# Kernel optimization log

Measured on AMD Instinct MI355X. Metric: run time of the kernel, lower is better.

The kernel has to match this reference:

```python
import jax, jax.numpy as jnp
import numpy as np

C = 2.0 + 1e-6
_nodes, _weights = np.polynomial.laguerre.laggauss(2)
QUAD_NODES = jnp.asarray(np.maximum(_nodes, 0.01) / C, dtype=jnp.float32)
QUAD_WEIGHTS = jnp.asarray(np.maximum(_weights, 0.01) / C, dtype=jnp.float32)
H, HD, P, M = 4, 64, 16, 32  # heads, head_dim, poly_dim, num_features
NUM_LABELS = 131072


def safe_normalize(x, axis=-1, eps=1e-4):
    n = jnp.linalg.norm(x, axis=axis, keepdims=True)
    return x / jnp.maximum(n, eps)


def safe_log(x, eps=1e-8):
    return jnp.log(jnp.maximum(x, eps))


def slay_features(x, omega, anchors):
    # x: [N, H*HD]; omega: [R,H,HD,M] (pre-scaled); anchors: [P,HD] (unit-norm)
    N = x.shape[0]
    xr = safe_normalize(x.reshape(N, H, HD), axis=-1)
    poly_proj = jnp.clip(jnp.einsum('nhd,pd->nhp', xr, anchors), -1.0, 1.0)
    poly_feat = poly_proj ** 2 / np.float32(np.sqrt(P))          # [N,H,P]
    prf_proj = jnp.einsum('nhd,rhdm->rnhm', xr, omega)           # [R,N,H,M]
    s = jnp.maximum(QUAD_NODES, 1e-6).reshape(-1, 1, 1, 1)
    exp_arg = jnp.clip(prf_proj * jnp.sqrt(2.0 * s) - s, -20.0, 20.0)
    prf_feat = jnp.exp(exp_arg) / np.float32(np.sqrt(M + 1e-6))
    prf_feat = prf_feat * jnp.sqrt(jnp.maximum(QUAD_WEIGHTS, 1e-6)).reshape(-1, 1, 1, 1)
    # fuse poly x prf, concat over quadrature nodes r (r-major feature order)
    fused = poly_feat[None, :, :, :, None] * prf_feat[:, :, :, None, :]  # [R,N,H,P,M]
    return fused.transpose(1, 0, 2, 3, 4).reshape(N, -1)         # [N, R*H*P*M]


def setup_inputs() -> dict:
    key = jax.random.key(0)
    ks = jax.random.split(key, 9)
    B, L, K = 1024, 128, 8
    return {
        'indices': jax.random.randint(ks[0], (B, L), 0, 100000),
        'mask': jnp.ones((B, L), dtype=jnp.float32),
        'labels': jax.random.randint(ks[1], (B, K), 0, NUM_LABELS),
        'label_mask': jnp.ones((B, K), dtype=jnp.float32),
        'neg_indices': jax.random.randint(ks[2], (2048,), 0, NUM_LABELS),
        'embed_table': jax.random.normal(ks[3], (100000, 256), dtype=jnp.float32),
        'kernel': jax.random.normal(ks[4], (256, NUM_LABELS), dtype=jnp.float32),
        'omega': jax.random.normal(ks[5], (2, H, HD, M), dtype=jnp.float32),
        'anchors': jax.random.normal(ks[6], (P, HD), dtype=jnp.float32),
    }


def reference(indices, mask, labels, label_mask, neg_indices, embed_table, kernel, omega, anchors):
    B, K = labels.shape
    # init-time parameter normalizations from the module
    omega_n = omega / np.float32(np.sqrt(HD))
    anchors_n = anchors / jnp.linalg.norm(anchors, axis=-1, keepdims=True)
    # MeanEmbedding encoder
    embeds = embed_table[indices]                                 # [B,L,D]
    summed = jnp.sum(embeds * mask[:, :, None], axis=1)
    query = summed / jnp.maximum(jnp.sum(mask, axis=1, keepdims=True), 1.0)
    query = safe_normalize(query, axis=-1)
    phi_query = slay_features(query, omega_n, anchors_n)          # [B,F]
    # sampled classifier rows
    W = safe_normalize(kernel.T, axis=-1)                         # [num_labels,D]
    safe_labels = jnp.maximum(labels, 0)
    all_needed = jnp.concatenate([safe_labels.reshape(-1), neg_indices])  # [B*K+Nneg]
    W_subset = W[all_needed]
    phi_W = slay_features(W_subset, omega_n, anchors_n)           # [B*K+Nneg,F]
    scores = phi_query @ phi_W.T                                  # [B, B*K+Nneg]
    idx_offsets = jnp.arange(B)[:, None] * K + jnp.arange(K)[None, :]
    pos_scores = jnp.take_along_axis(scores, idx_offsets, axis=1) # [B,K]
    neg_scores = scores[:, B * K:]                                # [B,Nneg]
    all_scores = jnp.concatenate([pos_scores, neg_scores], axis=1) + 1e-8
    log_Z = jax.scipy.special.logsumexp(safe_log(all_scores), axis=1)
    log_probs = safe_log(pos_scores + 1e-8) - log_Z[:, None]
    return -jnp.sum(log_probs * label_mask) / (jnp.sum(label_mask) + 1e-6)
```

## Files before the change

### kernel.cpp

```cpp
#include <hip/hip_runtime.h>
#include <math.h>

#define B_Q 1024
#define L_SEQ 128
#define D_EMB 256
#define NLAB 131072
#define LBL_ROWS 8192
#define NEG_ROWS 2048
#define W_ROWS 10240
#define CROW 320
#define LST 82
#define RPB 32
#define SXS 258

__device__ __forceinline__ float wave_sum(float v) {
#pragma unroll
  for (int off = 32; off > 0; off >>= 1) v += __shfl_xor(v, off, 64);
  return v;
}

__device__ __forceinline__ void slay_tail(const float* __restrict__ sx, int t,
                                          const float* __restrict__ anchT,
                                          const float* __restrict__ omega,
                                          float* __restrict__ outrow) {
  if (t < 64) {
    const int h = t >> 4, p = t & 15;
    const float* x = sx + h * 64;
    float d = 0.f;
#pragma unroll
    for (int dd = 0; dd < 64; dd++) d = fmaf(x[dd], anchT[dd * 16 + p], d);
    d = fminf(fmaxf(d, -1.0f), 1.0f);
    outrow[h * 16 + p] = d * d * 0.25f;
  }
  {
    const int r = t >> 7;
    const int h = (t >> 5) & 3;
    const float* x = sx + h * 64;
    const float* om = omega + (size_t)(t >> 5) * 2048 + (t & 31);
    float d = 0.f;
#pragma unroll
    for (int dd = 0; dd < 64; dd++) d = fmaf(x[dd], om[dd * 32], d);
    const float proj = d * 0.125f;
    const float s = r ? 1.70710592763316f : 0.29289307236691f;
    const float w = r ? 0.07322326809171f : 0.42677648190829f;
    float arg = proj * sqrtf(2.0f * s) - s;
    arg = fminf(fmaxf(arg, -20.0f), 20.0f);
    outrow[64 + t] = expf(arg) * (sqrtf(w) / sqrtf(32.000001f));
  }
}

__global__ __launch_bounds__(256) void k_setup(const float* __restrict__ anchors,
                                               const int* __restrict__ labels,
                                               const int* __restrict__ negidx,
                                               float* __restrict__ anchT,
                                               float* __restrict__ negparts,
                                               int* __restrict__ jidx,
                                               int* __restrict__ sorted) {
  __shared__ int shist[2048];
  __shared__ int s2[256];
  const int t = threadIdx.x, bx = blockIdx.x;
  if (bx == 0) {
    if (t < 64) {
      for (int p = 0; p < 16; p++) {
        const float v = anchors[p * 64 + t];
        const float n = sqrtf(wave_sum(v * v));
        anchT[t * 16 + p] = v / n;
      }
    }
  } else if (bx <= 256) {
    negparts[(bx - 1) * 256 + t] = 0.f;
  } else {
    for (int i = t; i < 2048; i += 256) shist[i] = 0;
    __syncthreads();
    int4 lv[8], nv[2];
#pragma unroll
    for (int e = 0; e < 8; e++) {
      int4 v = ((const int4*)labels)[e * 256 + t];
      v.x = max(v.x, 0); v.y = max(v.y, 0); v.z = max(v.z, 0); v.w = max(v.w, 0);
      lv[e] = v;
      ((int4*)jidx)[e * 256 + t] = v;
      atomicAdd(&shist[v.x >> 6], 1); atomicAdd(&shist[v.y >> 6], 1);
      atomicAdd(&shist[v.z >> 6], 1); atomicAdd(&shist[v.w >> 6], 1);
    }
#pragma unroll
    for (int e = 0; e < 2; e++) {
      const int4 v = ((const int4*)negidx)[e * 256 + t];
      nv[e] = v;
      ((int4*)jidx)[2048 + e * 256 + t] = v;
      atomicAdd(&shist[v.x >> 6], 1); atomicAdd(&shist[v.y >> 6], 1);
      atomicAdd(&shist[v.z >> 6], 1); atomicAdd(&shist[v.w >> 6], 1);
    }
    __syncthreads();
    int v[8]; int sum = 0;
#pragma unroll
    for (int e = 0; e < 8; e++) { v[e] = shist[t * 8 + e]; sum += v[e]; }
    s2[t] = sum; __syncthreads();
    for (int off = 1; off < 256; off <<= 1) {
      const int x = s2[t];
      const int y = (t >= off) ? s2[t - off] : 0;
      __syncthreads();
      s2[t] = x + y;
      __syncthreads();
    }
    int run = s2[t] - sum;
#pragma unroll
    for (int e = 0; e < 8; e++) { shist[t * 8 + e] = run; run += v[e]; }
    __syncthreads();
#pragma unroll
    for (int e = 0; e < 8; e++) {
      const int i = (e * 256 + t) * 4;
      sorted[atomicAdd(&shist[lv[e].x >> 6], 1)] = i;
      sorted[atomicAdd(&shist[lv[e].y >> 6], 1)] = i + 1;
      sorted[atomicAdd(&shist[lv[e].z >> 6], 1)] = i + 2;
      sorted[atomicAdd(&shist[lv[e].w >> 6], 1)] = i + 3;
    }
#pragma unroll
    for (int e = 0; e < 2; e++) {
      const int i = LBL_ROWS + (e * 256 + t) * 4;
      sorted[atomicAdd(&shist[nv[e].x >> 6], 1)] = i;
      sorted[atomicAdd(&shist[nv[e].y >> 6], 1)] = i + 1;
      sorted[atomicAdd(&shist[nv[e].z >> 6], 1)] = i + 2;
      sorted[atomicAdd(&shist[nv[e].w >> 6], 1)] = i + 3;
    }
  }
}

__global__ __launch_bounds__(256, 4) void k_feat(const int* __restrict__ indices,
                                                 const float* __restrict__ mask,
                                                 const float* __restrict__ embed,
                                                 const float* __restrict__ kern,
                                                 const float* __restrict__ anchT,
                                                 const float* __restrict__ omega,
                                                 const int* __restrict__ jidx,
                                                 const int* __restrict__ sorted,
                                                 float* __restrict__ qcomp,
                                                 float* __restrict__ wcomp) {
  __shared__ __align__(16) float smem[9504];
  const int tid = threadIdx.x;

  if (blockIdx.x < B_Q) {
    const int b = blockIdx.x, t = tid;
    const int wv = t >> 6, ln = t & 63;
    int* sidx = (int*)smem;
    float* smask = smem + 128;
    float4* spart = (float4*)(smem + 256);
    float* smsum = smem + 1280;
    float* sx = smem + 1296;
    if (t < L_SEQ) { sidx[t] = indices[b * L_SEQ + t]; smask[t] = mask[b * L_SEQ + t]; }
    __syncthreads();
    float4 acc = {0.f, 0.f, 0.f, 0.f};
    float msum = 0.f;
#pragma unroll 8
    for (int l = wv * 32; l < wv * 32 + 32; l++) {
      const float m = smask[l];
      msum += m;
      const float4 e = *(const float4*)(embed + (size_t)sidx[l] * D_EMB + ln * 4);
      acc.x = fmaf(e.x, m, acc.x); acc.y = fmaf(e.y, m, acc.y);
      acc.z = fmaf(e.z, m, acc.z); acc.w = fmaf(e.w, m, acc.w);
    }
    spart[wv * 64 + ln] = acc;
    if (ln == 0) smsum[wv] = msum;
    __syncthreads();
    const float* spf = (const float*)spart;
    float q = spf[t] + spf[256 + t] + spf[512 + t] + spf[768 + t];
    const float mt = smsum[0] + smsum[1] + smsum[2] + smsum[3];
    q /= fmaxf(mt, 1.0f);
    const float ss = wave_sum(q * q);
    sx[t] = q / fmaxf(sqrtf(ss), 1e-4f);
    __syncthreads();
    slay_tail(sx, t, anchT, omega, qcomp + (size_t)b * CROW);
  } else {
    const int lb = blockIdx.x - B_Q;
    int* sj = (int*)smem;
    int* ssid = (int*)smem + 32;
    float* rnorm = smem + 64;
    float* sq = smem + 192;
    float* sx = smem + 1248;
    const int cb = (lb & 7) * 40 + (lb >> 3);
    const int i0 = cb * RPB;

    if (tid < RPB) {
      const int sid = sorted[i0 + tid];
      ssid[tid] = sid;
      sj[tid] = jidx[sid];
    }
    __syncthreads();

    {
      const int row = tid & 31, dloc = tid >> 5;
      const float* kbase = kern + ((size_t)dloc << 17) + (size_t)sj[row];
      float ssq[4] = {0.f, 0.f, 0.f, 0.f};
#pragma unroll
      for (int it = 0; it < 32; it++) {
        const float v = kbase[(size_t)it << 20];
        sx[row * SXS + it * 8 + dloc] = v;
        ssq[it >> 3] = fmaf(v, v, ssq[it >> 3]);
      }
#pragma unroll
      for (int h = 0; h < 4; h++) sq[row * 33 + dloc * 4 + h] = ssq[h];
    }
    __syncthreads();
    if (tid < 128) {
      const int r2 = tid >> 2, h = tid & 3;
      float s = 0.f;
#pragma unroll
      for (int dl = 0; dl < 8; dl++) s += sq[r2 * 33 + dl * 4 + h];
      rnorm[r2 * 4 + h] = 1.0f / fmaxf(sqrtf(s), 1e-4f);
    }
    __syncthreads();

    {
      const int hh = (tid >> 5) & 3, r = tid >> 7;
      const float* om = omega + (size_t)(tid >> 5) * 2048 + (tid & 31);
      const float s = r ? 1.70710592763316f : 0.29289307236691f;
      const float w = r ? 0.07322326809171f : 0.42677648190829f;
      const float sc = sqrtf(2.0f * s);
      const float outs = sqrtf(w) / sqrtf(32.000001f);
#pragma unroll
      for (int half = 0; half < 2; half++) {
        float acc[16];
#pragma unroll
        for (int rq = 0; rq < 16; rq++) acc[rq] = 0.f;
#pragma unroll
        for (int dd = 0; dd < 64; dd += 2) {
          const float o0 = om[dd * 32], o1 = om[dd * 32 + 32];
#pragma unroll
          for (int rq = 0; rq < 16; rq++) {
            const float2 xv = *(const float2*)(sx + (half * 16 + rq) * SXS + hh * 64 + dd);
            acc[rq] = fmaf(xv.x, o0, fmaf(xv.y, o1, acc[rq]));
          }
        }
#pragma unroll
        for (int rq = 0; rq < 16; rq++) {
          const int row = half * 16 + rq;
          float arg = acc[rq] * 0.125f * rnorm[row * 4 + hh] * sc - s;
          arg = fminf(fmaxf(arg, -20.0f), 20.0f);
          wcomp[(size_t)ssid[row] * CROW + 64 + tid] = expf(arg) * outs;
        }
      }
    }

    {
      const int hp = tid & 63, rp = tid >> 6;
      const int h = hp >> 4, p = hp & 15;
#pragma unroll
      for (int pr = 0; pr < 4; pr++) {
        const int r0 = rp * 8 + pr * 2;
        const float* x0 = sx + r0 * SXS + h * 64;
        const float* x1 = x0 + SXS;
        float d0 = 0.f, d1 = 0.f;
#pragma unroll
        for (int dd = 0; dd < 64; dd++) {
          const float a = anchT[dd * 16 + p];
          d0 = fmaf(x0[dd], a, d0);
          d1 = fmaf(x1[dd], a, d1);
        }
        d0 *= rnorm[r0 * 4 + h];
        d1 *= rnorm[(r0 + 1) * 4 + h];
        d0 = fminf(fmaxf(d0, -1.0f), 1.0f);
        d1 = fminf(fmaxf(d1, -1.0f), 1.0f);
        wcomp[(size_t)ssid[r0] * CROW + h * 16 + p]     = d0 * d0 * 0.25f;
        wcomp[(size_t)ssid[r0 + 1] * CROW + h * 16 + p] = d1 * d1 * 0.25f;
      }
    }
  }
}

__global__ __launch_bounds__(128) void k_score(const float* __restrict__ qcomp,
                                               const float* __restrict__ wcomp,
                                               float* __restrict__ negparts,
                                               float* __restrict__ pos) {
  __shared__ float qt[64 * LST];
  __shared__ float wt[32 * LST];
  const int tid = threadIdx.x;

  if (blockIdx.x < 4096) {
    const int qb0 = (blockIdx.x & 15) * 64;
    const int wb  = (blockIdx.x >> 4) & 63;
    const int wr0 = LBL_ROWS + wb * 32;
    const int h   = blockIdx.x >> 10;

    for (int idx = tid; idx < 96 * 20; idx += 128) {
      const int row = idx / 20, c4 = idx % 20;
      int col, lcol;
      if (c4 < 4)       { col = h * 16 + c4 * 4;              lcol = c4 * 4; }
      else if (c4 < 12) { col = 64 + h * 32 + (c4 - 4) * 4;   lcol = 16 + (c4 - 4) * 4; }
      else              { col = 192 + h * 32 + (c4 - 12) * 4; lcol = 48 + (c4 - 12) * 4; }
      const bool isq = row < 64;
      const int grow = isq ? (qb0 + row) : (wr0 + row - 64);
      const float4 v = *(const float4*)((isq ? qcomp : wcomp) + (size_t)grow * CROW + col);
      float* dst = (isq ? qt + row * LST : wt + (row - 64) * LST) + lcol;
      dst[0] = v.x; dst[1] = v.y; dst[2] = v.z; dst[3] = v.w;
    }
    __syncthreads();

    const int qg = tid >> 3;
    const int wg = tid & 7;
    const float* qb = qt + (qg * 4) * LST;
    const float* wbp = wt + (wg * 4) * LST;

    float pd[4][4] = {{0.f}}, pf[4][4] = {{0.f}};
#pragma unroll
    for (int kc = 0; kc < 8; kc++) {
      float2 qv[4], wv[4];
#pragma unroll
      for (int i = 0; i < 4; i++) qv[i] = *(const float2*)(qb + i * LST + 2 * kc);
#pragma unroll
      for (int j = 0; j < 4; j++) wv[j] = *(const float2*)(wbp + j * LST + 2 * kc);
#pragma unroll
      for (int i = 0; i < 4; i++)
#pragma unroll
        for (int j = 0; j < 4; j++) {
          pd[i][j] = fmaf(qv[i].x, wv[j].x, pd[i][j]);
          pd[i][j] = fmaf(qv[i].y, wv[j].y, pd[i][j]);
        }
    }
#pragma unroll 8
    for (int kc = 0; kc < 32; kc++) {
      float2 qv[4], wv[4];
#pragma unroll
      for (int i = 0; i < 4; i++) qv[i] = *(const float2*)(qb + i * LST + 16 + 2 * kc);
#pragma unroll
      for (int j = 0; j < 4; j++) wv[j] = *(const float2*)(wbp + j * LST + 16 + 2 * kc);
#pragma unroll
      for (int i = 0; i < 4; i++)
#pragma unroll
        for (int j = 0; j < 4; j++) {
          pf[i][j] = fmaf(qv[i].x, wv[j].x, pf[i][j]);
          pf[i][j] = fmaf(qv[i].y, wv[j].y, pf[i][j]);
        }
    }

#pragma unroll
    for (int i = 0; i < 4; i++) {
      float acc = 0.f;
#pragma unroll
      for (int j = 0; j < 4; j++) acc += pd[i][j] * pf[i][j];
#pragma unroll
      for (int off = 1; off < 8; off <<= 1) acc += __shfl_xor(acc, off, 64);
      if (wg == 0) atomicAdd(&negparts[wb * B_Q + qb0 + qg * 4 + i], acc);
    }
  } else {
    const int g = (blockIdx.x - 4096) * 32 + (tid >> 2);
    const int h = tid & 3;
    const float* q = qcomp + (size_t)(g >> 3) * CROW;
    const float* w = wcomp + (size_t)g * CROW;
    float pd = 0.f, pf = 0.f;
#pragma unroll
    for (int c = 0; c < 4; c++) {
      const float4 qv = *(const float4*)(q + h * 16 + c * 4);
      const float4 wv = *(const float4*)(w + h * 16 + c * 4);
      pd += qv.x * wv.x + qv.y * wv.y + qv.z * wv.z + qv.w * wv.w;
    }
#pragma unroll
    for (int r = 0; r < 2; r++)
#pragma unroll
      for (int c = 0; c < 8; c++) {
        const float4 qv = *(const float4*)(q + 64 + r * 128 + h * 32 + c * 4);
        const float4 wv = *(const float4*)(w + 64 + r * 128 + h * 32 + c * 4);
        pf += qv.x * wv.x + qv.y * wv.y + qv.z * wv.z + qv.w * wv.w;
      }
    float sc = pd * pf;
    sc += __shfl_xor(sc, 1, 64);
    sc += __shfl_xor(sc, 2, 64);
    if (h == 0) pos[g] = sc;
  }
}

__global__ __launch_bounds__(1024) void k_loss(const float* __restrict__ pos,
                                               const float* __restrict__ negparts,
                                               const float* __restrict__ lmask,
                                               float* __restrict__ out) {
  const int b = threadIdx.x;
  float lp[8];
  float possum = 0.f;
#pragma unroll
  for (int k = 0; k < 8; k++) { lp[k] = pos[b * 8 + k]; possum += lp[k]; }
  float negsum = 0.f;
#pragma unroll 8
  for (int c = 0; c < 64; c++) negsum += negparts[c * B_Q + b];
  const float Z = possum + negsum + 2.056e-5f;
  const float logZ = logf(Z);
  float local = 0.f, lsum = 0.f;
#pragma unroll
  for (int k = 0; k < 8; k++) {
    const float lm = lmask[b * 8 + k];
    local += lm * (logf(lp[k] + 1e-8f) - logZ);
    lsum += lm;
  }
  local = wave_sum(local);
  lsum = wave_sum(lsum);
  __shared__ float r1[16], r2[16];
  const int wid = b >> 6;
  if ((b & 63) == 0) { r1[wid] = local; r2[wid] = lsum; }
  __syncthreads();
  if (b == 0) {
    float t1 = 0.f, t2 = 0.f;
    for (int wv = 0; wv < 16; wv++) { t1 += r1[wv]; t2 += r2[wv]; }
    out[0] = -t1 / (t2 + 1e-6f);
  }
}

extern "C" void kernel_launch(void* const* d_in, const int* in_sizes, int n_in,
                              void* d_out, int out_size, void* d_ws, size_t ws_size,
                              hipStream_t stream) {
  const int* indices  = (const int*)d_in[0];
  const float* mask   = (const float*)d_in[1];
  const int* labels   = (const int*)d_in[2];
  const float* lmask  = (const float*)d_in[3];
  const int* negidx   = (const int*)d_in[4];
  const float* embed  = (const float*)d_in[5];
  const float* kern   = (const float*)d_in[6];
  const float* omega  = (const float*)d_in[7];
  const float* anchors= (const float*)d_in[8];
  float* out = (float*)d_out;

  float* ws = (float*)d_ws;
  float* anchT    = ws;
  float* qcomp    = anchT + 1024;
  float* wcomp    = qcomp + (size_t)B_Q * CROW;
  float* pos      = wcomp + (size_t)W_ROWS * CROW;
  float* negparts = pos + LBL_ROWS;
  int*   jidx     = (int*)(negparts + 64 * B_Q);
  int*   sorted   = jidx + W_ROWS;

  k_setup<<<258, 256, 0, stream>>>(anchors, labels, negidx, anchT, negparts, jidx, sorted);
  k_feat<<<B_Q + W_ROWS / RPB, 256, 0, stream>>>(indices, mask, embed, kern, anchT, omega,
                                                 jidx, sorted, qcomp, wcomp);
  k_score<<<4096 + 256, 128, 0, stream>>>(qcomp, wcomp, negparts, pos);
  k_loss<<<1, 1024, 0, stream>>>(pos, negparts, lmask, out);
}
```

Measured before the change: 355.2 us.

## Stream full classifier kernel coalesced and scatter needed columns into a compact buffer

The old fused setup and feature kernels are split into a prep/mark/scan/scatter pipeline that builds a label-to-slot map, deduplicating repeated labels with atomicMin. A new gather kernel reads the whole 256x131072 kernel matrix with coalesced float4 loads and scatters only the needed columns into a dense W_ROWS-wide buffer. The projection kernel then reads from that compact buffer instead of issuing strided 4-byte gathers across the large matrix. The aim is to replace latency-bound scattered reads with sequential bandwidth-bound streaming. In exchange it reads the entire matrix and adds several extra kernel launches plus workspace for the gathered columns and slot map.

Measured after the change: 391.5 us. 10.2% more time.

```diff
diff --git a/kernel.cpp b/kernel.cpp
--- a/kernel.cpp
+++ b/kernel.cpp
@@ -12,6 +12,7 @@
 #define LST 82
 #define RPB 32
 #define SXS 258
+#define SLOT_EMPTY 0x7FFFFFFF
 
 __device__ __forceinline__ float wave_sum(float v) {
 #pragma unroll
@@ -49,15 +50,11 @@
   }
 }
 
-__global__ __launch_bounds__(256) void k_setup(const float* __restrict__ anchors,
-                                               const int* __restrict__ labels,
-                                               const int* __restrict__ negidx,
-                                               float* __restrict__ anchT,
-                                               float* __restrict__ negparts,
-                                               int* __restrict__ jidx,
-                                               int* __restrict__ sorted) {
-  __shared__ int shist[2048];
-  __shared__ int s2[256];
+__global__ __launch_bounds__(256) void k_prep(const float* __restrict__ anchors,
+                                              float* __restrict__ anchT,
+                                              float* __restrict__ negparts,
+                                              int* __restrict__ hist,
+                                              int* __restrict__ slotmap) {
   const int t = threadIdx.x, bx = blockIdx.x;
   if (bx == 0) {
     if (t < 64) {
@@ -69,77 +66,85 @@
     }
   } else if (bx <= 256) {
     negparts[(bx - 1) * 256 + t] = 0.f;
+  } else if (bx <= 264) {
+    hist[(bx - 257) * 256 + t] = 0;
   } else {
-    for (int i = t; i < 2048; i += 256) shist[i] = 0;
-    __syncthreads();
-    int4 lv[8], nv[2];
-#pragma unroll
-    for (int e = 0; e < 8; e++) {
-      int4 v = ((const int4*)labels)[e * 256 + t];
-      v.x = max(v.x, 0); v.y = max(v.y, 0); v.z = max(v.z, 0); v.w = max(v.w, 0);
-      lv[e] = v;
-      ((int4*)jidx)[e * 256 + t] = v;
-      atomicAdd(&shist[v.x >> 6], 1); atomicAdd(&shist[v.y >> 6], 1);
-      atomicAdd(&shist[v.z >> 6], 1); atomicAdd(&shist[v.w >> 6], 1);
-    }
-#pragma unroll
-    for (int e = 0; e < 2; e++) {
-      const int4 v = ((const int4*)negidx)[e * 256 + t];
-      nv[e] = v;
-      ((int4*)jidx)[2048 + e * 256 + t] = v;
-      atomicAdd(&shist[v.x >> 6], 1); atomicAdd(&shist[v.y >> 6], 1);
-      atomicAdd(&shist[v.z >> 6], 1); atomicAdd(&shist[v.w >> 6], 1);
-    }
-    __syncthreads();
-    int v[8]; int sum = 0;
-#pragma unroll
-    for (int e = 0; e < 8; e++) { v[e] = shist[t * 8 + e]; sum += v[e]; }
-    s2[t] = sum; __syncthreads();
-    for (int off = 1; off < 256; off <<= 1) {
-      const int x = s2[t];
-      const int y = (t >= off) ? s2[t - off] : 0;
-      __syncthreads();
-      s2[t] = x + y;
-      __syncthreads();
-    }
-    int run = s2[t] - sum;
-#pragma unroll
-    for (int e = 0; e < 8; e++) { shist[t * 8 + e] = run; run += v[e]; }
-    __syncthreads();
-#pragma unroll
-    for (int e = 0; e < 8; e++) {
-      const int i = (e * 256 + t) * 4;
-      sorted[atomicAdd(&shist[lv[e].x >> 6], 1)] = i;
-      sorted[atomicAdd(&shist[lv[e].y >> 6], 1)] = i + 1;
-      sorted[atomicAdd(&shist[lv[e].z >> 6], 1)] = i + 2;
-      sorted[atomicAdd(&shist[lv[e].w >> 6], 1)] = i + 3;
-    }
-#pragma unroll
-    for (int e = 0; e < 2; e++) {
-      const int i = LBL_ROWS + (e * 256 + t) * 4;
-      sorted[atomicAdd(&shist[nv[e].x >> 6], 1)] = i;
-      sorted[atomicAdd(&shist[nv[e].y >> 6], 1)] = i + 1;
-      sorted[atomicAdd(&shist[nv[e].z >> 6], 1)] = i + 2;
-      sorted[atomicAdd(&shist[nv[e].w >> 6], 1)] = i + 3;
-    }
-  }
-}
-
-__global__ __launch_bounds__(256, 4) void k_feat(const int* __restrict__ indices,
-                                                 const float* __restrict__ mask,
-                                                 const float* __restrict__ embed,
-                                                 const float* __restrict__ kern,
-                                                 const float* __restrict__ anchT,
-                                                 const float* __restrict__ omega,
-                                                 const int* __restrict__ jidx,
-                                                 const int* __restrict__ sorted,
-                                                 float* __restrict__ qcomp,
-                                                 float* __restrict__ wcomp) {
-  __shared__ __align__(16) float smem[9504];
+    slotmap[(bx - 265) * 256 + t] = SLOT_EMPTY;
+  }
+}
+
+__global__ __launch_bounds__(256) void k_mark(const int* __restrict__ labels,
+                                              const int* __restrict__ negidx,
+                                              int* __restrict__ jidx,
+                                              int* __restrict__ hist) {
+  const int i = blockIdx.x * 256 + threadIdx.x;
+  if (i >= W_ROWS) return;
+  int j;
+  if (i < LBL_ROWS) { j = labels[i]; if (j < 0) j = 0; }
+  else               { j = negidx[i - LBL_ROWS]; }
+  jidx[i] = j;
+  atomicAdd(&hist[j >> 6], 1);
+}
+
+__global__ __launch_bounds__(256) void k_scan(int* __restrict__ hist) {
+  __shared__ int s[256];
+  const int t = threadIdx.x;
+  int v[8]; int sum = 0;
+#pragma unroll
+  for (int e = 0; e < 8; e++) { v[e] = hist[t * 8 + e]; sum += v[e]; }
+  s[t] = sum; __syncthreads();
+  for (int off = 1; off < 256; off <<= 1) {
+    const int x = s[t];
+    const int y = (t >= off) ? s[t - off] : 0;
+    __syncthreads();
+    s[t] = x + y;
+    __syncthreads();
+  }
+  int run = s[t] - sum;
+#pragma unroll
+  for (int e = 0; e < 8; e++) { hist[t * 8 + e] = run; run += v[e]; }
+}
+
+__global__ __launch_bounds__(256) void k_scatter(const int* __restrict__ jidx,
+                                                 int* __restrict__ hist,
+                                                 int* __restrict__ sorted,
+                                                 int* __restrict__ slotmap) {
+  const int i = blockIdx.x * 256 + threadIdx.x;
+  if (i >= W_ROWS) return;
+  const int j = jidx[i];
+  const int pos = atomicAdd(&hist[j >> 6], 1);
+  sorted[pos] = i;
+  atomicMin(&slotmap[j], pos);
+}
+
+__global__ __launch_bounds__(256) void k_gather(const float* __restrict__ kern,
+                                                const int* __restrict__ slotmap,
+                                                float* __restrict__ wgath,
+                                                const int* __restrict__ indices,
+                                                const float* __restrict__ mask,
+                                                const float* __restrict__ embed,
+                                                const float* __restrict__ anchT,
+                                                const float* __restrict__ omega,
+                                                float* __restrict__ qcomp) {
   const int tid = threadIdx.x;
-
-  if (blockIdx.x < B_Q) {
-    const int b = blockIdx.x, t = tid;
+  if (blockIdx.x < 2048) {
+    const int d = blockIdx.x >> 3, chunk = blockIdx.x & 7;
+    const float4* kb = (const float4*)(kern + ((size_t)d << 17)) + chunk * 4096;
+    const int4* sm = (const int4*)slotmap + chunk * 4096;
+    float* wg = wgath + (size_t)d * W_ROWS;
+#pragma unroll 4
+    for (int it = 0; it < 16; it++) {
+      const int idx = it * 256 + tid;
+      const float4 v = kb[idx];
+      const int4 s = sm[idx];
+      if (s.x < W_ROWS) wg[s.x] = v.x;
+      if (s.y < W_ROWS) wg[s.y] = v.y;
+      if (s.z < W_ROWS) wg[s.z] = v.z;
+      if (s.w < W_ROWS) wg[s.w] = v.w;
+    }
+  } else {
+    __shared__ __align__(16) float smem[1552];
+    const int b = blockIdx.x - 2048, t = tid;
     const int wv = t >> 6, ln = t & 63;
     int* sidx = (int*)smem;
     float* smask = smem + 128;
@@ -169,99 +174,112 @@
     sx[t] = q / fmaxf(sqrtf(ss), 1e-4f);
     __syncthreads();
     slay_tail(sx, t, anchT, omega, qcomp + (size_t)b * CROW);
-  } else {
-    const int lb = blockIdx.x - B_Q;
-    int* sj = (int*)smem;
-    int* ssid = (int*)smem + 32;
-    float* rnorm = smem + 64;
-    float* sq = smem + 192;
-    float* sx = smem + 1248;
-    const int cb = (lb & 7) * 40 + (lb >> 3);
-    const int i0 = cb * RPB;
-
-    if (tid < RPB) {
-      const int sid = sorted[i0 + tid];
-      ssid[tid] = sid;
-      sj[tid] = jidx[sid];
-    }
-    __syncthreads();
-
-    {
-      const int row = tid & 31, dloc = tid >> 5;
-      const float* kbase = kern + ((size_t)dloc << 17) + (size_t)sj[row];
-      float ssq[4] = {0.f, 0.f, 0.f, 0.f};
-#pragma unroll
-      for (int it = 0; it < 32; it++) {
-        const float v = kbase[(size_t)it << 20];
-        sx[row * SXS + it * 8 + dloc] = v;
-        ssq[it >> 3] = fmaf(v, v, ssq[it >> 3]);
-      }
-#pragma unroll
-      for (int h = 0; h < 4; h++) sq[row * 33 + dloc * 4 + h] = ssq[h];
-    }
-    __syncthreads();
-    if (tid < 128) {
-      const int r2 = tid >> 2, h = tid & 3;
-      float s = 0.f;
-#pragma unroll
-      for (int dl = 0; dl < 8; dl++) s += sq[r2 * 33 + dl * 4 + h];
-      rnorm[r2 * 4 + h] = 1.0f / fmaxf(sqrtf(s), 1e-4f);
-    }
-    __syncthreads();
-
-    {
-      const int hh = (tid >> 5) & 3, r = tid >> 7;
-      const float* om = omega + (size_t)(tid >> 5) * 2048 + (tid & 31);
-      const float s = r ? 1.70710592763316f : 0.29289307236691f;
-      const float w = r ? 0.07322326809171f : 0.42677648190829f;
-      const float sc = sqrtf(2.0f * s);
-      const float outs = sqrtf(w) / sqrtf(32.000001f);
-#pragma unroll
-      for (int half = 0; half < 2; half++) {
-        float acc[16];
-#pragma unroll
-        for (int rq = 0; rq < 16; rq++) acc[rq] = 0.f;
-#pragma unroll
-        for (int dd = 0; dd < 64; dd += 2) {
-          const float o0 = om[dd * 32], o1 = om[dd * 32 + 32];
-#pragma unroll
-          for (int rq = 0; rq < 16; rq++) {
-            const float2 xv = *(const float2*)(sx + (half * 16 + rq) * SXS + hh * 64 + dd);
-            acc[rq] = fmaf(xv.x, o0, fmaf(xv.y, o1, acc[rq]));
-          }
-        }
+  }
+}
+
+__global__ __launch_bounds__(256) void k_wproj(const int* __restrict__ sorted,
+                                               const int* __restrict__ jidx,
+                                               const int* __restrict__ slotmap,
+                                               const float* __restrict__ wgath,
+                                               const float* __restrict__ anchT,
+                                               const float* __restrict__ omega,
+                                               float* __restrict__ wcomp) {
+  __shared__ __align__(16) float smem[9536];
+  int* sj = (int*)smem;
+  int* ssid = (int*)smem + 32;
+  int* sslot = (int*)smem + 64;
+  float* rnorm = smem + 96;
+  float* sq = smem + 224;
+  float* sx = smem + 1280;
+  const int tid = threadIdx.x;
+  const int lb = blockIdx.x;
+  const int cb = (lb & 7) * 40 + (lb >> 3);
+  const int i0 = cb * RPB;
+
+  if (tid < RPB) {
+    const int sid = sorted[i0 + tid];
+    ssid[tid] = sid;
+    const int j = jidx[sid];
+    sj[tid] = j;
+    sslot[tid] = slotmap[j];
+  }
+  __syncthreads();
+
+  {
+    const int row = tid & 31, dloc = tid >> 5;
+    const float* wg = wgath + sslot[row];
+    float ssq[4] = {0.f, 0.f, 0.f, 0.f};
+#pragma unroll
+    for (int it = 0; it < 32; it++) {
+      const float v = wg[(size_t)(it * 8 + dloc) * W_ROWS];
+      sx[row * SXS + it * 8 + dloc] = v;
+      ssq[it >> 3] = fmaf(v, v, ssq[it >> 3]);
+    }
+#pragma unroll
+    for (int h = 0; h < 4; h++) sq[row * 33 + dloc * 4 + h] = ssq[h];
+  }
+  __syncthreads();
+  if (tid < 128) {
+    const int r2 = tid >> 2, h = tid & 3;
+    float s = 0.f;
+#pragma unroll
+    for (int dl = 0; dl < 8; dl++) s += sq[r2 * 33 + dl * 4 + h];
+    rnorm[r2 * 4 + h] = 1.0f / fmaxf(sqrtf(s), 1e-4f);
+  }
+  __syncthreads();
+
+  {
+    const int hh = (tid >> 5) & 3, r = tid >> 7;
+    const float* om = omega + (size_t)(tid >> 5) * 2048 + (tid & 31);
+    const float s = r ? 1.70710592763316f : 0.29289307236691f;
+    const float w = r ? 0.07322326809171f : 0.42677648190829f;
+    const float sc = sqrtf(2.0f * s);
+    const float outs = sqrtf(w) / sqrtf(32.000001f);
+#pragma unroll
+    for (int half = 0; half < 2; half++) {
+      float acc[16];
+#pragma unroll
+      for (int rq = 0; rq < 16; rq++) acc[rq] = 0.f;
+#pragma unroll
+      for (int dd = 0; dd < 64; dd += 2) {
+        const float o0 = om[dd * 32], o1 = om[dd * 32 + 32];
 #pragma unroll
         for (int rq = 0; rq < 16; rq++) {
-          const int row = half * 16 + rq;
-          float arg = acc[rq] * 0.125f * rnorm[row * 4 + hh] * sc - s;
-          arg = fminf(fmaxf(arg, -20.0f), 20.0f);
-          wcomp[(size_t)ssid[row] * CROW + 64 + tid] = expf(arg) * outs;
+          const float2 xv = *(const float2*)(sx + (half * 16 + rq) * SXS + hh * 64 + dd);
+          acc[rq] = fmaf(xv.x, o0, fmaf(xv.y, o1, acc[rq]));
         }
       }
-    }
-
-    {
-      const int hp = tid & 63, rp = tid >> 6;
-      const int h = hp >> 4, p = hp & 15;
-#pragma unroll
-      for (int pr = 0; pr < 4; pr++) {
-        const int r0 = rp * 8 + pr * 2;
-        const float* x0 = sx + r0 * SXS + h * 64;
-        const float* x1 = x0 + SXS;
-        float d0 = 0.f, d1 = 0.f;
-#pragma unroll
-        for (int dd = 0; dd < 64; dd++) {
-          const float a = anchT[dd * 16 + p];
-          d0 = fmaf(x0[dd], a, d0);
-          d1 = fmaf(x1[dd], a, d1);
-        }
-        d0 *= rnorm[r0 * 4 + h];
-        d1 *= rnorm[(r0 + 1) * 4 + h];
-        d0 = fminf(fmaxf(d0, -1.0f), 1.0f);
-        d1 = fminf(fmaxf(d1, -1.0f), 1.0f);
-        wcomp[(size_t)ssid[r0] * CROW + h * 16 + p]     = d0 * d0 * 0.25f;
-        wcomp[(size_t)ssid[r0 + 1] * CROW + h * 16 + p] = d1 * d1 * 0.25f;
+#pragma unroll
+      for (int rq = 0; rq < 16; rq++) {
+        const int row = half * 16 + rq;
+        float arg = acc[rq] * 0.125f * rnorm[row * 4 + hh] * sc - s;
+        arg = fminf(fmaxf(arg, -20.0f), 20.0f);
+        wcomp[(size_t)ssid[row] * CROW + 64 + tid] = expf(arg) * outs;
       }
+    }
+  }
+
+  {
+    const int hp = tid & 63, rp = tid >> 6;
+    const int h = hp >> 4, p = hp & 15;
+#pragma unroll
+    for (int pr = 0; pr < 4; pr++) {
+      const int r0 = rp * 8 + pr * 2;
+      const float* x0 = sx + r0 * SXS + h * 64;
+      const float* x1 = x0 + SXS;
+      float d0 = 0.f, d1 = 0.f;
+#pragma unroll
+      for (int dd = 0; dd < 64; dd++) {
+        const float a = anchT[dd * 16 + p];
+        d0 = fmaf(x0[dd], a, d0);
+        d1 = fmaf(x1[dd], a, d1);
+      }
+      d0 *= rnorm[r0 * 4 + h];
+      d1 *= rnorm[(r0 + 1) * 4 + h];
+      d0 = fminf(fmaxf(d0, -1.0f), 1.0f);
+      d1 = fminf(fmaxf(d1, -1.0f), 1.0f);
+      wcomp[(size_t)ssid[r0] * CROW + h * 16 + p]     = d0 * d0 * 0.25f;
+      wcomp[(size_t)ssid[r0 + 1] * CROW + h * 16 + p] = d1 * d1 * 0.25f;
     }
   }
 }
@@ -419,14 +437,21 @@
   float* anchT    = ws;
   float* qcomp    = anchT + 1024;
   float* wcomp    = qcomp + (size_t)B_Q * CROW;
-  float* pos      = wcomp + (size_t)W_ROWS * CROW;
+  float* wgath    = wcomp + (size_t)W_ROWS * CROW;
+  float* pos      = wgath + (size_t)D_EMB * W_ROWS;
   float* negparts = pos + LBL_ROWS;
   int*   jidx     = (int*)(negparts + 64 * B_Q);
   int*   sorted   = jidx + W_ROWS;
-
-  k_setup<<<258, 256, 0, stream>>>(anchors, labels, negidx, anchT, negparts, jidx, sorted);
-  k_feat<<<B_Q + W_ROWS / RPB, 256, 0, stream>>>(indices, mask, embed, kern, anchT, omega,
-                                                 jidx, sorted, qcomp, wcomp);
+  int*   hist     = sorted + W_ROWS;
+  int*   slotmap  = hist + 2048;
+
+  k_prep<<<777, 256, 0, stream>>>(anchors, anchT, negparts, hist, slotmap);
+  k_mark<<<40, 256, 0, stream>>>(labels, negidx, jidx, hist);
+  k_scan<<<1, 256, 0, stream>>>(hist);
+  k_scatter<<<40, 256, 0, stream>>>(jidx, hist, sorted, slotmap);
+  k_gather<<<3072, 256, 0, stream>>>(kern, slotmap, wgath, indices, mask, embed,
+                                     anchT, omega, qcomp);
+  k_wproj<<<W_ROWS / RPB, 256, 0, stream>>>(sorted, jidx, slotmap, wgath, anchT, omega, wcomp);
   k_score<<<4096 + 256, 128, 0, stream>>>(qcomp, wcomp, negparts, pos);
   k_loss<<<1, 1024, 0, stream>>>(pos, negparts, lmask, out);
 }
```

## Retile negative scoring to 128x64 blocks looping heads, dropping atomics

Applied to the files above, without the earlier changes.

The negative-score kernel now uses 256-thread blocks that each cover 128 queries by 64 negative rows and loop over all four heads inside the block. Each thread keeps an 8x4 register tile, and the W tile is stored transposed in shared memory. Per-head products are accumulated in registers, so each partial is written with a plain store instead of an atomicAdd, and the zero-fill of negparts in setup is removed. The goal is more data reuse and register blocking, plus fewer launches and atomics, at the cost of a much smaller grid (384 blocks) and higher register pressure.

New measurement: 357.1 us. Within noise of the previous version (+0.6%).

```diff
diff --git a/kernel.cpp b/kernel.cpp
--- a/kernel.cpp
+++ b/kernel.cpp
@@ -9,9 +9,10 @@
 #define NEG_ROWS 2048
 #define W_ROWS 10240
 #define CROW 320
-#define LST 82
 #define RPB 32
 #define SXS 258
+#define QST 84
+#define NWT 32
 
 __device__ __forceinline__ float wave_sum(float v) {
 #pragma unroll
@@ -53,7 +54,6 @@
                                                const int* __restrict__ labels,
                                                const int* __restrict__ negidx,
                                                float* __restrict__ anchT,
-                                               float* __restrict__ negparts,
                                                int* __restrict__ jidx,
                                                int* __restrict__ sorted) {
   __shared__ int shist[2048];
@@ -67,8 +67,6 @@
         anchT[t * 16 + p] = v / n;
       }
     }
-  } else if (bx <= 256) {
-    negparts[(bx - 1) * 256 + t] = 0.f;
   } else {
     for (int i = t; i < 2048; i += 256) shist[i] = 0;
     __syncthreads();
@@ -266,82 +264,110 @@
   }
 }
 
-__global__ __launch_bounds__(128) void k_score(const float* __restrict__ qcomp,
+__global__ __launch_bounds__(256) void k_score(const float* __restrict__ qcomp,
                                                const float* __restrict__ wcomp,
                                                float* __restrict__ negparts,
                                                float* __restrict__ pos) {
-  __shared__ float qt[64 * LST];
-  __shared__ float wt[32 * LST];
+  __shared__ __align__(16) float sq[128 * QST];
+  __shared__ __align__(16) float swt[80 * 64];
   const int tid = threadIdx.x;
 
-  if (blockIdx.x < 4096) {
-    const int qb0 = (blockIdx.x & 15) * 64;
-    const int wb  = (blockIdx.x >> 4) & 63;
-    const int wr0 = LBL_ROWS + wb * 32;
-    const int h   = blockIdx.x >> 10;
-
-    for (int idx = tid; idx < 96 * 20; idx += 128) {
-      const int row = idx / 20, c4 = idx % 20;
-      int col, lcol;
-      if (c4 < 4)       { col = h * 16 + c4 * 4;              lcol = c4 * 4; }
-      else if (c4 < 12) { col = 64 + h * 32 + (c4 - 4) * 4;   lcol = 16 + (c4 - 4) * 4; }
-      else              { col = 192 + h * 32 + (c4 - 12) * 4; lcol = 48 + (c4 - 12) * 4; }
-      const bool isq = row < 64;
-      const int grow = isq ? (qb0 + row) : (wr0 + row - 64);
-      const float4 v = *(const float4*)((isq ? qcomp : wcomp) + (size_t)grow * CROW + col);
-      float* dst = (isq ? qt + row * LST : wt + (row - 64) * LST) + lcol;
-      dst[0] = v.x; dst[1] = v.y; dst[2] = v.z; dst[3] = v.w;
-    }
-    __syncthreads();
-
-    const int qg = tid >> 3;
-    const int wg = tid & 7;
-    const float* qb = qt + (qg * 4) * LST;
-    const float* wbp = wt + (wg * 4) * LST;
-
-    float pd[4][4] = {{0.f}}, pf[4][4] = {{0.f}};
-#pragma unroll
-    for (int kc = 0; kc < 8; kc++) {
-      float2 qv[4], wv[4];
-#pragma unroll
-      for (int i = 0; i < 4; i++) qv[i] = *(const float2*)(qb + i * LST + 2 * kc);
-#pragma unroll
-      for (int j = 0; j < 4; j++) wv[j] = *(const float2*)(wbp + j * LST + 2 * kc);
-#pragma unroll
-      for (int i = 0; i < 4; i++)
-#pragma unroll
-        for (int j = 0; j < 4; j++) {
-          pd[i][j] = fmaf(qv[i].x, wv[j].x, pd[i][j]);
-          pd[i][j] = fmaf(qv[i].y, wv[j].y, pd[i][j]);
+  if (blockIdx.x < 256) {
+    const int qt = blockIdx.x & 7;
+    const int wb = blockIdx.x >> 3;
+    const int q0 = qt * 128;
+    const int wr0 = LBL_ROWS + wb * 64;
+    const int qg = tid >> 4;
+    const int wg = tid & 15;
+
+    float acc[8][4];
+#pragma unroll
+    for (int i = 0; i < 8; i++)
+#pragma unroll
+      for (int j = 0; j < 4; j++) acc[i][j] = 0.f;
+
+    for (int h = 0; h < 4; h++) {
+#pragma unroll
+      for (int k = 0; k < 10; k++) {
+        const int idx = k * 256 + tid;
+        const int row = idx / 20, c4 = idx % 20;
+        int col;
+        if (c4 < 4)       col = h * 16 + c4 * 4;
+        else if (c4 < 12) col = 64 + h * 32 + (c4 - 4) * 4;
+        else              col = 192 + h * 32 + (c4 - 12) * 4;
+        const float4 v = *(const float4*)(qcomp + (size_t)(q0 + row) * CROW + col);
+        *(float4*)(sq + row * QST + c4 * 4) = v;
+      }
+#pragma unroll
+      for (int k = 0; k < 5; k++) {
+        const int idx = k * 256 + tid;
+        const int row = idx / 20, c4 = idx % 20;
+        int col;
+        if (c4 < 4)       col = h * 16 + c4 * 4;
+        else if (c4 < 12) col = 64 + h * 32 + (c4 - 4) * 4;
+        else              col = 192 + h * 32 + (c4 - 12) * 4;
+        const float4 v = *(const float4*)(wcomp + (size_t)(wr0 + row) * CROW + col);
+        swt[(c4 * 4 + 0) * 64 + row] = v.x;
+        swt[(c4 * 4 + 1) * 64 + row] = v.y;
+        swt[(c4 * 4 + 2) * 64 + row] = v.z;
+        swt[(c4 * 4 + 3) * 64 + row] = v.w;
+      }
+      __syncthreads();
+
+      float pd[8][4], pf[8][4];
+#pragma unroll
+      for (int i = 0; i < 8; i++)
+#pragma unroll
+        for (int j = 0; j < 4; j++) { pd[i][j] = 0.f; pf[i][j] = 0.f; }
+
+#pragma unroll
+      for (int c = 0; c < 20; c++) {
+        float4 qv[8];
+#pragma unroll
+        for (int i = 0; i < 8; i++)
+          qv[i] = *(const float4*)(sq + (qg * 8 + i) * QST + c * 4);
+#pragma unroll
+        for (int k = 0; k < 4; k++) {
+          const float4 wvk = *(const float4*)(swt + (c * 4 + k) * 64 + wg * 4);
+          if (c < 4) {
+#pragma unroll
+            for (int i = 0; i < 8; i++) {
+              const float qik = ((const float*)&qv[i])[k];
+              pd[i][0] = fmaf(qik, wvk.x, pd[i][0]);
+              pd[i][1] = fmaf(qik, wvk.y, pd[i][1]);
+              pd[i][2] = fmaf(qik, wvk.z, pd[i][2]);
+              pd[i][3] = fmaf(qik, wvk.w, pd[i][3]);
+            }
+          } else {
+#pragma unroll
+            for (int i = 0; i < 8; i++) {
+              const float qik = ((const float*)&qv[i])[k];
+              pf[i][0] = fmaf(qik, wvk.x, pf[i][0]);
+              pf[i][1] = fmaf(qik, wvk.y, pf[i][1]);
+              pf[i][2] = fmaf(qik, wvk.z, pf[i][2]);
+              pf[i][3] = fmaf(qik, wvk.w, pf[i][3]);
+            }
+          }
         }
-    }
-#pragma unroll 8
-    for (int kc = 0; kc < 32; kc++) {
-      float2 qv[4], wv[4];
-#pragma unroll
-      for (int i = 0; i < 4; i++) qv[i] = *(const float2*)(qb + i * LST + 16 + 2 * kc);
-#pragma unroll
-      for (int j = 0; j < 4; j++) wv[j] = *(const float2*)(wbp + j * LST + 16 + 2 * kc);
-#pragma unroll
-      for (int i = 0; i < 4; i++)
-#pragma unroll
-        for (int j = 0; j < 4; j++) {
-          pf[i][j] = fmaf(qv[i].x, wv[j].x, pf[i][j]);
-          pf[i][j] = fmaf(qv[i].y, wv[j].y, pf[i][j]);
-        }
-    }
-
-#pragma unroll
-    for (int i = 0; i < 4; i++) {
-      float acc = 0.f;
-#pragma unroll
-      for (int j = 0; j < 4; j++) acc += pd[i][j] * pf[i][j];
-#pragma unroll
-      for (int off = 1; off < 8; off <<= 1) acc += __shfl_xor(acc, off, 64);
-      if (wg == 0) atomicAdd(&negparts[wb * B_Q + qb0 + qg * 4 + i], acc);
+      }
+#pragma unroll
+      for (int i = 0; i < 8; i++)
+#pragma unroll
+        for (int j = 0; j < 4; j++) acc[i][j] = fmaf(pd[i][j], pf[i][j], acc[i][j]);
+      __syncthreads();
+    }
+
+#pragma unroll
+    for (int i = 0; i < 8; i++) {
+      float r = acc[i][0] + acc[i][1] + acc[i][2] + acc[i][3];
+      r += __shfl_xor(r, 1, 64);
+      r += __shfl_xor(r, 2, 64);
+      r += __shfl_xor(r, 4, 64);
+      r += __shfl_xor(r, 8, 64);
+      if (wg == 0) negparts[wb * B_Q + q0 + qg * 8 + i] = r;
     }
   } else {
-    const int g = (blockIdx.x - 4096) * 32 + (tid >> 2);
+    const int g = (blockIdx.x - 256) * 64 + (tid >> 2);
     const int h = tid & 3;
     const float* q = qcomp + (size_t)(g >> 3) * CROW;
     const float* w = wcomp + (size_t)g * CROW;
@@ -378,7 +404,7 @@
   for (int k = 0; k < 8; k++) { lp[k] = pos[b * 8 + k]; possum += lp[k]; }
   float negsum = 0.f;
 #pragma unroll 8
-  for (int c = 0; c < 64; c++) negsum += negparts[c * B_Q + b];
+  for (int c = 0; c < NWT; c++) negsum += negparts[c * B_Q + b];
   const float Z = possum + negsum + 2.056e-5f;
   const float logZ = logf(Z);
   float local = 0.f, lsum = 0.f;
@@ -421,12 +447,12 @@
   float* wcomp    = qcomp + (size_t)B_Q * CROW;
   float* pos      = wcomp + (size_t)W_ROWS * CROW;
   float* negparts = pos + LBL_ROWS;
-  int*   jidx     = (int*)(negparts + 64 * B_Q);
+  int*   jidx     = (int*)(negparts + NWT * B_Q);
   int*   sorted   = jidx + W_ROWS;
 
-  k_setup<<<258, 256, 0, stream>>>(anchors, labels, negidx, anchT, negparts, jidx, sorted);
+  k_setup<<<2, 256, 0, stream>>>(anchors, labels, negidx, anchT, jidx, sorted);
   k_feat<<<B_Q + W_ROWS / RPB, 256, 0, stream>>>(indices, mask, embed, kern, anchT, omega,
                                                  jidx, sorted, qcomp, wcomp);
-  k_score<<<4096 + 256, 128, 0, stream>>>(qcomp, wcomp, negparts, pos);
+  k_score<<<256 + 128, 256, 0, stream>>>(qcomp, wcomp, negparts, pos);
   k_loss<<<1, 1024, 0, stream>>>(pos, negparts, lmask, out);
 }
```
